# Kernel optimization log

Hardware: AMD Instinct MI355X
Metric: run time of the kernel (lower is better)

Reference implementation:

```python
import jax, jax.numpy as jnp
import numpy as np

N_NODES = 50000
N_EDGES = 800000
N_FEAT, N_HID, N_LATENT = 512, 256, 128


def spmm(rows, cols, vals, dense):
    # out[r] += vals[e] * dense[cols[e]]  -- COO SpMM via segment_sum
    gathered = dense[cols] * vals[:, None]          # [E, d]
    return jax.ops.segment_sum(gathered, rows, num_segments=N_NODES)


def setup_inputs() -> dict:
    key = jax.random.key(0)
    ks = jax.random.split(key, 8)
    x = jax.random.normal(ks[0], (N_NODES, N_FEAT), dtype=jnp.float32)
    edge_rows = jax.random.randint(ks[1], (N_EDGES,), 0, N_NODES, dtype=jnp.int32)
    edge_cols = jax.random.randint(ks[2], (N_EDGES,), 0, N_NODES, dtype=jnp.int32)
    edge_vals = jax.random.uniform(ks[3], (N_EDGES,), dtype=jnp.float32)
    # Glorot-style init like the torch GraphConvolution
    W1 = jax.random.normal(ks[4], (N_FEAT, N_HID), dtype=jnp.float32) / np.sqrt(N_FEAT)
    b1 = jnp.zeros((N_HID,), dtype=jnp.float32)
    W2 = jax.random.normal(ks[5], (N_HID, N_LATENT), dtype=jnp.float32) / np.sqrt(N_HID)
    b2 = jnp.zeros((N_LATENT,), dtype=jnp.float32)
    return {"x": x, "edge_rows": edge_rows, "edge_cols": edge_cols,
            "edge_vals": edge_vals, "W1": W1, "b1": b1, "W2": W2, "b2": b2}


def reference(x, edge_rows, edge_cols, edge_vals, W1, b1, W2, b2):
    # layer 1: relu(adj @ (x @ W1) + b1)
    h = spmm(edge_rows, edge_cols, edge_vals, x @ W1) + b1
    h = jax.nn.relu(h)
    # layer 2: relu(adj @ (h @ W2) + b2)
    z = spmm(edge_rows, edge_cols, edge_vals, h @ W2) + b2
    return jax.nn.relu(z)
```

## Files before the change

### kernel.cpp

```cpp
#include <hip/hip_runtime.h>
#include <hip/hip_bf16.h>


typedef __attribute__((ext_vector_type(8))) short bf16x8;
typedef __attribute__((ext_vector_type(8))) unsigned short ushort8;
typedef __attribute__((ext_vector_type(4))) float f32x4;

#define NN 50000
#define NE 800000
#define NF 512
#define NH 256
#define NL 128
#define NB ((NN + 255) / 256)

static __device__ __forceinline__ unsigned short f2bf(float f) {
  union { float f; unsigned int u; } v; v.f = f;
  unsigned int r = v.u + 0x7fffu + ((v.u >> 16) & 1u);
  return (unsigned short)(r >> 16);
}
static __device__ __forceinline__ float bf2f(unsigned short u) {
  union { unsigned int u; float f; } v; v.u = (unsigned int)u << 16;
  return v.f;
}

static __device__ __forceinline__ void gll16(const void* g, void* l) {
  __builtin_amdgcn_global_load_lds(
      (const __attribute__((address_space(1))) void*)g,
      (__attribute__((address_space(3))) void*)l, 16, 0, 0);
}

extern "C" __global__ void k_hist(const int* __restrict__ rows, int* __restrict__ counts, int n) {
  int i = blockIdx.x * 256 + threadIdx.x;
  if (i < n) atomicAdd(&counts[rows[i]], 1);
}

extern "C" __global__ __launch_bounds__(256) void k_blocksum(
    const int* __restrict__ counts, int* __restrict__ bsum, int n) {
  __shared__ int s[256];
  int t = threadIdx.x;
  int i = blockIdx.x * 256 + t;
  s[t] = (i < n) ? counts[i] : 0;
  __syncthreads();
  for (int off = 128; off > 0; off >>= 1) {
    if (t < off) s[t] += s[t + off];
    __syncthreads();
  }
  if (t == 0) bsum[blockIdx.x] = s[0];
}

extern "C" __global__ __launch_bounds__(256) void k_scansums(
    const int* __restrict__ bsum, int* __restrict__ bpre, int* __restrict__ rp, int nb, int n) {
  __shared__ int s[256];
  int t = threadIdx.x;
  int v = (t < nb) ? bsum[t] : 0;
  s[t] = v;
  __syncthreads();
  for (int off = 1; off < 256; off <<= 1) {
    int u = (t >= off) ? s[t - off] : 0;
    __syncthreads();
    s[t] += u;
    __syncthreads();
  }
  if (t < nb) bpre[t] = s[t] - v;
  if (t == 255) rp[n] = s[255];
}

extern "C" __global__ __launch_bounds__(256) void k_scanfin(
    const int* __restrict__ counts, const int* __restrict__ bpre,
    int* __restrict__ rp, int* __restrict__ cur, int n) {
  __shared__ int s[256];
  int t = threadIdx.x;
  int i = blockIdx.x * 256 + t;
  int c = (i < n) ? counts[i] : 0;
  s[t] = c;
  __syncthreads();
  for (int off = 1; off < 256; off <<= 1) {
    int u = (t >= off) ? s[t - off] : 0;
    __syncthreads();
    s[t] += u;
    __syncthreads();
  }
  if (i < n) {
    int e = bpre[blockIdx.x] + s[t] - c;
    rp[i] = e;
    cur[i] = e;
  }
}

extern "C" __global__ void k_scatter(const int* __restrict__ rows, const int* __restrict__ cols,
    const float* __restrict__ vals, int* __restrict__ cur, int2* __restrict__ ep, int n) {
  int i = blockIdx.x * 256 + threadIdx.x;
  if (i < n) {
    int p = atomicAdd(&cur[rows[i]], 1);
    int2 e; e.x = cols[i]; e.y = __float_as_int(vals[i]);
    ep[p] = e;
  }
}

extern "C" __global__ void k_transcast(const float* __restrict__ w, unsigned short* __restrict__ wt,
                                       int K, int N) {
  int k = blockIdx.x; int n = threadIdx.x;
  wt[(size_t)n * K + k] = f2bf(w[(size_t)k * N + n]);
}

extern "C" __global__ __launch_bounds__(256) void k_gemm1(
    const float* __restrict__ A, const unsigned short* __restrict__ BT,
    unsigned short* __restrict__ C) {
  __shared__ __align__(16) unsigned short sA[128 * 64];
  __shared__ __align__(16) unsigned short sB[128 * 64];
  int tid = threadIdx.x;
  int lane = tid & 63, wid = tid >> 6;
  int wm = (wid >> 1) * 64, wn = (wid & 1) * 64;
  int bm = blockIdx.x * 128, bn = blockIdx.y * 128;
  int l15 = lane & 15, lq = lane >> 4;
  int swzbase = l15 & 7;
  f32x4 acc[4][4];
#pragma unroll
  for (int i = 0; i < 4; ++i)
#pragma unroll
    for (int j = 0; j < 4; ++j) acc[i][j] = (f32x4){0.f, 0.f, 0.f, 0.f};

  for (int k0 = 0; k0 < NF; k0 += 64) {
#pragma unroll
    for (int j = 0; j < 4; ++j) {
      int u = tid + 256 * j;
      int row = u >> 3, cu = u & 7;
      int ga = bm + row; if (ga >= NN) ga = NN - 1;
      const float* src = A + (size_t)ga * NF + k0 + cu * 8;
      float4 f0 = *(const float4*)src;
      float4 f1 = *(const float4*)(src + 4);
      ushort8 o;
      o[0] = f2bf(f0.x); o[1] = f2bf(f0.y); o[2] = f2bf(f0.z); o[3] = f2bf(f0.w);
      o[4] = f2bf(f1.x); o[5] = f2bf(f1.y); o[6] = f2bf(f1.z); o[7] = f2bf(f1.w);
      *(ushort8*)(&sA[row * 64 + (cu ^ (row & 7)) * 8]) = o;
    }
#pragma unroll
    for (int j = 0; j < 4; ++j) {
      int u = tid + 256 * j;
      int row = u >> 3, cu = u & 7;
      int g = cu ^ (row & 7);
      gll16(BT + (size_t)(bn + row) * NF + k0 + g * 8, &sB[u * 8]);
    }
    __syncthreads();
#pragma unroll
    for (int ks = 0; ks < 64; ks += 32) {
      bf16x8 af[4], bfr[4];
#pragma unroll
      for (int t = 0; t < 4; ++t) {
        int sz = (((ks >> 3) + lq) ^ swzbase) * 8;
        af[t]  = *(const bf16x8*)(&sA[(wm + t * 16 + l15) * 64 + sz]);
        bfr[t] = *(const bf16x8*)(&sB[(wn + t * 16 + l15) * 64 + sz]);
      }
#pragma unroll
      for (int mt = 0; mt < 4; ++mt)
#pragma unroll
        for (int nt = 0; nt < 4; ++nt)
          acc[mt][nt] = __builtin_amdgcn_mfma_f32_16x16x32_bf16(af[mt], bfr[nt], acc[mt][nt], 0, 0, 0);
    }
    __syncthreads();
  }
#pragma unroll
  for (int mt = 0; mt < 4; ++mt) {
#pragma unroll
    for (int r = 0; r < 4; ++r) {
      int gr = bm + wm + mt * 16 + lq * 4 + r;
      if (gr < NN) {
#pragma unroll
        for (int nt = 0; nt < 4; ++nt) {
          int gc = bn + wn + nt * 16 + l15;
          C[(size_t)gr * NH + gc] = f2bf(acc[mt][nt][r]);
        }
      }
    }
  }
}

extern "C" __global__ __launch_bounds__(256) void k_gemm2(
    const unsigned short* __restrict__ A, const unsigned short* __restrict__ BT,
    unsigned short* __restrict__ C) {
  __shared__ __align__(16) unsigned short sA[64 * 64];
  __shared__ __align__(16) unsigned short sB[128 * 64];
  int tid = threadIdx.x;
  int lane = tid & 63, wid = tid >> 6;
  int wm = (wid >> 1) * 32, wn = (wid & 1) * 64;
  int bm = blockIdx.x * 64;
  int l15 = lane & 15, lq = lane >> 4;
  int swzbase = l15 & 7;
  f32x4 acc[2][4];
#pragma unroll
  for (int i = 0; i < 2; ++i)
#pragma unroll
    for (int j = 0; j < 4; ++j) acc[i][j] = (f32x4){0.f, 0.f, 0.f, 0.f};

  for (int k0 = 0; k0 < NH; k0 += 64) {
#pragma unroll
    for (int j = 0; j < 2; ++j) {
      int u = tid + 256 * j;
      int row = u >> 3, cu = u & 7;
      int ga = bm + row; if (ga >= NN) ga = NN - 1;
      int g = cu ^ (row & 7);
      gll16(A + (size_t)ga * NH + k0 + g * 8, &sA[u * 8]);
    }
#pragma unroll
    for (int j = 0; j < 4; ++j) {
      int u = tid + 256 * j;
      int row = u >> 3, cu = u & 7;
      int g = cu ^ (row & 7);
      gll16(BT + (size_t)row * NH + k0 + g * 8, &sB[u * 8]);
    }
    __syncthreads();
#pragma unroll
    for (int ks = 0; ks < 64; ks += 32) {
      bf16x8 af[2], bfr[4];
#pragma unroll
      for (int t = 0; t < 2; ++t)
        af[t] = *(const bf16x8*)(&sA[(wm + t * 16 + l15) * 64 + (((ks >> 3) + lq) ^ swzbase) * 8]);
#pragma unroll
      for (int t = 0; t < 4; ++t)
        bfr[t] = *(const bf16x8*)(&sB[(wn + t * 16 + l15) * 64 + (((ks >> 3) + lq) ^ swzbase) * 8]);
#pragma unroll
      for (int mt = 0; mt < 2; ++mt)
#pragma unroll
        for (int nt = 0; nt < 4; ++nt)
          acc[mt][nt] = __builtin_amdgcn_mfma_f32_16x16x32_bf16(af[mt], bfr[nt], acc[mt][nt], 0, 0, 0);
    }
    __syncthreads();
  }
#pragma unroll
  for (int mt = 0; mt < 2; ++mt) {
#pragma unroll
    for (int r = 0; r < 4; ++r) {
      int gr = bm + wm + mt * 16 + lq * 4 + r;
      if (gr < NN) {
#pragma unroll
        for (int nt = 0; nt < 4; ++nt) {
          int gc = wn + nt * 16 + l15;
          C[(size_t)gr * NL + gc] = f2bf(acc[mt][nt][r]);
        }
      }
    }
  }
}

extern "C" __global__ __launch_bounds__(256) void k_spmm256(
    const int* __restrict__ rp, const int2* __restrict__ ep,
    const unsigned short* __restrict__ src, const float* __restrict__ bias,
    ushort4* __restrict__ out) {
  int row = blockIdx.x * 4 + (threadIdx.x >> 6);
  int lane = threadIdx.x & 63;
  if (row >= NN) return;
  int e0 = __builtin_amdgcn_readfirstlane(rp[row]);
  int e1 = __builtin_amdgcn_readfirstlane(rp[row + 1]);
  const ushort4* srcv = (const ushort4*)src;
  float4 acc = {0.f, 0.f, 0.f, 0.f};
  int e = e0;
  for (; e + 8 <= e1; e += 8) {
    int2 p[8]; ushort4 g[8];
#pragma unroll
    for (int j = 0; j < 8; ++j) p[j] = ep[e + j];
#pragma unroll
    for (int j = 0; j < 8; ++j) g[j] = srcv[(size_t)p[j].x * (NH / 4) + lane];
#pragma unroll
    for (int j = 0; j < 8; ++j) {
      float v = __int_as_float(p[j].y);
      acc.x = fmaf(v, bf2f(g[j].x), acc.x); acc.y = fmaf(v, bf2f(g[j].y), acc.y);
      acc.z = fmaf(v, bf2f(g[j].z), acc.z); acc.w = fmaf(v, bf2f(g[j].w), acc.w);
    }
  }
  for (; e + 4 <= e1; e += 4) {
    int2 p[4]; ushort4 g[4];
#pragma unroll
    for (int j = 0; j < 4; ++j) p[j] = ep[e + j];
#pragma unroll
    for (int j = 0; j < 4; ++j) g[j] = srcv[(size_t)p[j].x * (NH / 4) + lane];
#pragma unroll
    for (int j = 0; j < 4; ++j) {
      float v = __int_as_float(p[j].y);
      acc.x = fmaf(v, bf2f(g[j].x), acc.x); acc.y = fmaf(v, bf2f(g[j].y), acc.y);
      acc.z = fmaf(v, bf2f(g[j].z), acc.z); acc.w = fmaf(v, bf2f(g[j].w), acc.w);
    }
  }
  for (; e < e1; ++e) {
    int2 p = ep[e];
    float v = __int_as_float(p.y);
    ushort4 g = srcv[(size_t)p.x * (NH / 4) + lane];
    acc.x = fmaf(v, bf2f(g.x), acc.x); acc.y = fmaf(v, bf2f(g.y), acc.y);
    acc.z = fmaf(v, bf2f(g.z), acc.z); acc.w = fmaf(v, bf2f(g.w), acc.w);
  }
  float4 b = ((const float4*)bias)[lane];
  ushort4 o;
  o.x = f2bf(fmaxf(acc.x + b.x, 0.f));
  o.y = f2bf(fmaxf(acc.y + b.y, 0.f));
  o.z = f2bf(fmaxf(acc.z + b.z, 0.f));
  o.w = f2bf(fmaxf(acc.w + b.w, 0.f));
  out[(size_t)row * (NH / 4) + lane] = o;
}

extern "C" __global__ __launch_bounds__(256) void k_spmm128(
    const int* __restrict__ rp, const int2* __restrict__ ep,
    const unsigned short* __restrict__ src, const float* __restrict__ bias,
    float2* __restrict__ out) {
  int row = blockIdx.x * 4 + (threadIdx.x >> 6);
  int lane = threadIdx.x & 63;
  if (row >= NN) return;
  int e0 = __builtin_amdgcn_readfirstlane(rp[row]);
  int e1 = __builtin_amdgcn_readfirstlane(rp[row + 1]);
  const ushort2* srcv = (const ushort2*)src;
  float2 acc = {0.f, 0.f};
  int e = e0;
  for (; e + 8 <= e1; e += 8) {
    int2 p[8]; ushort2 g[8];
#pragma unroll
    for (int j = 0; j < 8; ++j) p[j] = ep[e + j];
#pragma unroll
    for (int j = 0; j < 8; ++j) g[j] = srcv[(size_t)p[j].x * (NL / 2) + lane];
#pragma unroll
    for (int j = 0; j < 8; ++j) {
      float v = __int_as_float(p[j].y);
      acc.x = fmaf(v, bf2f(g[j].x), acc.x); acc.y = fmaf(v, bf2f(g[j].y), acc.y);
    }
  }
  for (; e + 4 <= e1; e += 4) {
    int2 p[4]; ushort2 g[4];
#pragma unroll
    for (int j = 0; j < 4; ++j) p[j] = ep[e + j];
#pragma unroll
    for (int j = 0; j < 4; ++j) g[j] = srcv[(size_t)p[j].x * (NL / 2) + lane];
#pragma unroll
    for (int j = 0; j < 4; ++j) {
      float v = __int_as_float(p[j].y);
      acc.x = fmaf(v, bf2f(g[j].x), acc.x); acc.y = fmaf(v, bf2f(g[j].y), acc.y);
    }
  }
  for (; e < e1; ++e) {
    int2 p = ep[e];
    float v = __int_as_float(p.y);
    ushort2 g = srcv[(size_t)p.x * (NL / 2) + lane];
    acc.x = fmaf(v, bf2f(g.x), acc.x); acc.y = fmaf(v, bf2f(g.y), acc.y);
  }
  float2 b = ((const float2*)bias)[lane];
  float2 o;
  o.x = fmaxf(acc.x + b.x, 0.f);
  o.y = fmaxf(acc.y + b.y, 0.f);
  out[(size_t)row * (NL / 2) + lane] = o;
}

extern "C" void kernel_launch(void* const* d_in, const int* in_sizes, int n_in,
                              void* d_out, int out_size, void* d_ws, size_t ws_size,
                              hipStream_t stream) {
  const float* x   = (const float*)d_in[0];
  const int* erow  = (const int*)d_in[1];
  const int* ecol  = (const int*)d_in[2];
  const float* ev  = (const float*)d_in[3];
  const float* W1  = (const float*)d_in[4];
  const float* b1  = (const float*)d_in[5];
  const float* W2  = (const float*)d_in[6];
  const float* b2  = (const float*)d_in[7];

  char* ws = (char*)d_ws;
  unsigned short* xwb = (unsigned short*)(ws + 0);
  unsigned short* hbf = (unsigned short*)(ws + 25600000);
  unsigned short* hwb = (unsigned short*)(ws + 51200000);
  unsigned short* w1t = (unsigned short*)(ws + 64000000);
  unsigned short* w2t = (unsigned short*)(ws + 64262144);
  int* rp    = (int*)(ws + 64327680);
  int* cur   = (int*)(ws + 64528384);
  int* cnt   = (int*)(ws + 64729088);
  int* bsum  = (int*)(ws + 64929792);
  int* bpre  = (int*)(ws + 64930816);
  int2* ep   = (int2*)(ws + 64931840);

  hipMemsetAsync(cnt, 0, NN * sizeof(int), stream);
  k_hist<<<NE / 256, 256, 0, stream>>>(erow, cnt, NE);
  k_blocksum<<<NB, 256, 0, stream>>>(cnt, bsum, NN);
  k_scansums<<<1, 256, 0, stream>>>(bsum, bpre, rp, NB, NN);
  k_scanfin<<<NB, 256, 0, stream>>>(cnt, bpre, rp, cur, NN);
  k_scatter<<<NE / 256, 256, 0, stream>>>(erow, ecol, ev, cur, ep, NE);

  k_transcast<<<NF, NH, 0, stream>>>(W1, w1t, NF, NH);
  k_gemm1<<<dim3((NN + 127) / 128, NH / 128), 256, 0, stream>>>(x, w1t, xwb);
  k_spmm256<<<NN / 4, 256, 0, stream>>>(rp, ep, xwb, b1, (ushort4*)hbf);

  k_transcast<<<NH, NL, 0, stream>>>(W2, w2t, NH, NL);
  k_gemm2<<<(NN + 63) / 64, 256, 0, stream>>>(hbf, w2t, hwb);
  k_spmm128<<<NN / 4, 256, 0, stream>>>(rp, ep, hwb, b2, (float2*)d_out);
}
```

Before: 375.4 us.

## Register-prefetch next K tile in both GEMMs to overlap loads with MFMA

Both GEMM kernels now prefetch the next K-slice of A and B into registers right after the barrier, then write them to LDS at the top of the next iteration. This replaces direct global-to-LDS loads and the load-then-wait pattern, so global latency overlaps with the MFMA loop. It also switches the fp32-to-bf16 conversion to a packed intrinsic and sets a minimum occupancy of 3 blocks per CU on gemm1. The cost is higher register pressure from the prefetch buffers, which the occupancy hint may force into spills.

```diff
diff --git a/kernel.cpp b/kernel.cpp
--- a/kernel.cpp
+++ b/kernel.cpp
@@ -3,7 +3,6 @@
 
 
 typedef __attribute__((ext_vector_type(8))) short bf16x8;
-typedef __attribute__((ext_vector_type(8))) unsigned short ushort8;
 typedef __attribute__((ext_vector_type(4))) float f32x4;
 
 #define NN 50000
@@ -22,11 +21,10 @@
   union { unsigned int u; float f; } v; v.u = (unsigned int)u << 16;
   return v.f;
 }
-
-static __device__ __forceinline__ void gll16(const void* g, void* l) {
-  __builtin_amdgcn_global_load_lds(
-      (const __attribute__((address_space(1))) void*)g,
-      (__attribute__((address_space(3))) void*)l, 16, 0, 0);
+static __device__ __forceinline__ unsigned int pk2bf(float a, float b) {
+  __hip_bfloat162 h = __float22bfloat162_rn(make_float2(a, b));
+  union { __hip_bfloat162 h; unsigned int u; } v; v.h = h;
+  return v.u;
 }
 
 extern "C" __global__ void k_hist(const int* __restrict__ rows, int* __restrict__ counts, int n) {
@@ -103,7 +101,7 @@
   wt[(size_t)n * K + k] = f2bf(w[(size_t)k * N + n]);
 }
 
-extern "C" __global__ __launch_bounds__(256) void k_gemm1(
+extern "C" __global__ __launch_bounds__(256, 3) void k_gemm1(
     const float* __restrict__ A, const unsigned short* __restrict__ BT,
     unsigned short* __restrict__ C) {
   __shared__ __align__(16) unsigned short sA[128 * 64];
@@ -120,28 +118,51 @@
 #pragma unroll
     for (int j = 0; j < 4; ++j) acc[i][j] = (f32x4){0.f, 0.f, 0.f, 0.f};
 
+  int arow[4], acu[4];
+  const float* aptr[4];
+  const unsigned short* bptr[4];
+  unsigned int asw[4], bsw[4];
+#pragma unroll
+  for (int j = 0; j < 4; ++j) {
+    int u = tid + 256 * j;
+    int row = u >> 3, cu = u & 7;
+    arow[j] = row; acu[j] = cu;
+    int ga = bm + row; if (ga >= NN) ga = NN - 1;
+    aptr[j] = A + (size_t)ga * NF + cu * 8;
+    bptr[j] = BT + (size_t)(bn + row) * NF + cu * 8;
+    asw[j] = row * 64 + (cu ^ (row & 7)) * 8;
+    bsw[j] = asw[j];
+  }
+
+  float4 pa[4][2];
+  bf16x8 pb[4];
+#pragma unroll
+  for (int j = 0; j < 4; ++j) {
+    pa[j][0] = *(const float4*)(aptr[j]);
+    pa[j][1] = *(const float4*)(aptr[j] + 4);
+    pb[j] = *(const bf16x8*)(bptr[j]);
+  }
+
   for (int k0 = 0; k0 < NF; k0 += 64) {
 #pragma unroll
     for (int j = 0; j < 4; ++j) {
-      int u = tid + 256 * j;
-      int row = u >> 3, cu = u & 7;
-      int ga = bm + row; if (ga >= NN) ga = NN - 1;
-      const float* src = A + (size_t)ga * NF + k0 + cu * 8;
-      float4 f0 = *(const float4*)src;
-      float4 f1 = *(const float4*)(src + 4);
-      ushort8 o;
-      o[0] = f2bf(f0.x); o[1] = f2bf(f0.y); o[2] = f2bf(f0.z); o[3] = f2bf(f0.w);
-      o[4] = f2bf(f1.x); o[5] = f2bf(f1.y); o[6] = f2bf(f1.z); o[7] = f2bf(f1.w);
-      *(ushort8*)(&sA[row * 64 + (cu ^ (row & 7)) * 8]) = o;
-    }
-#pragma unroll
-    for (int j = 0; j < 4; ++j) {
-      int u = tid + 256 * j;
-      int row = u >> 3, cu = u & 7;
-      int g = cu ^ (row & 7);
-      gll16(BT + (size_t)(bn + row) * NF + k0 + g * 8, &sB[u * 8]);
-    }
-    __syncthreads();
+      uint4 o;
+      o.x = pk2bf(pa[j][0].x, pa[j][0].y);
+      o.y = pk2bf(pa[j][0].z, pa[j][0].w);
+      o.z = pk2bf(pa[j][1].x, pa[j][1].y);
+      o.w = pk2bf(pa[j][1].z, pa[j][1].w);
+      *(uint4*)(&sA[asw[j]]) = o;
+      *(bf16x8*)(&sB[bsw[j]]) = pb[j];
+    }
+    __syncthreads();
+    if (k0 + 64 < NF) {
+#pragma unroll
+      for (int j = 0; j < 4; ++j) {
+        pa[j][0] = *(const float4*)(aptr[j] + k0 + 64);
+        pa[j][1] = *(const float4*)(aptr[j] + k0 + 64 + 4);
+        pb[j] = *(const bf16x8*)(bptr[j] + k0 + 64);
+      }
+    }
 #pragma unroll
     for (int ks = 0; ks < 64; ks += 32) {
       bf16x8 af[4], bfr[4];
@@ -192,23 +213,43 @@
 #pragma unroll
     for (int j = 0; j < 4; ++j) acc[i][j] = (f32x4){0.f, 0.f, 0.f, 0.f};
 
+  const unsigned short* aptr[2];
+  const unsigned short* bptr[4];
+  unsigned int asw[2], bsw[4];
+#pragma unroll
+  for (int j = 0; j < 2; ++j) {
+    int u = tid + 256 * j;
+    int row = u >> 3, cu = u & 7;
+    int ga = bm + row; if (ga >= NN) ga = NN - 1;
+    aptr[j] = A + (size_t)ga * NH + cu * 8;
+    asw[j] = row * 64 + (cu ^ (row & 7)) * 8;
+  }
+#pragma unroll
+  for (int j = 0; j < 4; ++j) {
+    int u = tid + 256 * j;
+    int row = u >> 3, cu = u & 7;
+    bptr[j] = BT + (size_t)row * NH + cu * 8;
+    bsw[j] = row * 64 + (cu ^ (row & 7)) * 8;
+  }
+
+  bf16x8 pA[2], pB[4];
+#pragma unroll
+  for (int j = 0; j < 2; ++j) pA[j] = *(const bf16x8*)(aptr[j]);
+#pragma unroll
+  for (int j = 0; j < 4; ++j) pB[j] = *(const bf16x8*)(bptr[j]);
+
   for (int k0 = 0; k0 < NH; k0 += 64) {
 #pragma unroll
-    for (int j = 0; j < 2; ++j) {
-      int u = tid + 256 * j;
-      int row = u >> 3, cu = u & 7;
-      int ga = bm + row; if (ga >= NN) ga = NN - 1;
-      int g = cu ^ (row & 7);
-      gll16(A + (size_t)ga * NH + k0 + g * 8, &sA[u * 8]);
-    }
-#pragma unroll
-    for (int j = 0; j < 4; ++j) {
-      int u = tid + 256 * j;
-      int row = u >> 3, cu = u & 7;
-      int g = cu ^ (row & 7);
-      gll16(BT + (size_t)row * NH + k0 + g * 8, &sB[u * 8]);
-    }
-    __syncthreads();
+    for (int j = 0; j < 2; ++j) *(bf16x8*)(&sA[asw[j]]) = pA[j];
+#pragma unroll
+    for (int j = 0; j < 4; ++j) *(bf16x8*)(&sB[bsw[j]]) = pB[j];
+    __syncthreads();
+    if (k0 + 64 < NH) {
+#pragma unroll
+      for (int j = 0; j < 2; ++j) pA[j] = *(const bf16x8*)(aptr[j] + k0 + 64);
+#pragma unroll
+      for (int j = 0; j < 4; ++j) pB[j] = *(const bf16x8*)(bptr[j] + k0 + 64);
+    }
 #pragma unroll
     for (int ks = 0; ks < 64; ks += 32) {
       bf16x8 af[2], bfr[4];
```

New measurement: 378.4 us. No clear change (+0.8%).
